# Performance work log

Measured on AMD Instinct MI355X. Metric: run time of the kernel, lower is better.

Reference implementation:

```python
import jax, jax.numpy as jnp
import numpy as np

NUM_ENTITIES = 100000
NUM_RELATIONS = 1000
BATCH = 65536
NUM_NEGS = 64
NUM_TRUE = 1000000


def _hash_triples(t):
    # matches torch: h = e0 << 42 | r << 21 | e2 (ids < 2^21 so no overlap)
    t = t.astype(jnp.int64)
    return (t[:, 0] << 42) | (t[:, 1] << 21) | t[:, 2]


def setup_inputs() -> dict:
    key = jax.random.key(0)
    k1, k2, k3, k4, k5 = jax.random.split(key, 5)
    # positive triples: entities in [1, NUM_ENTITIES), relations in [0, NUM_RELATIONS)
    heads = jax.random.randint(k1, (BATCH,), 1, NUM_ENTITIES, dtype=jnp.int64)
    rels = jax.random.randint(k2, (BATCH,), 0, NUM_RELATIONS, dtype=jnp.int64)
    tails = jax.random.randint(k3, (BATCH,), 1, NUM_ENTITIES, dtype=jnp.int64)
    positive_batch = jnp.stack([heads, rels, tails], axis=1)
    total = BATCH * NUM_NEGS
    # pre-drawn uniform candidates in [1, NUM_ENTITIES) (pad_idx=0 excluded by construction)
    rand_vals = jax.random.randint(k4, (total,), 1, NUM_ENTITIES, dtype=jnp.int64)
    # filter table: sorted unique hashes of training triples (built on host, like buffer init)
    rng = np.random.default_rng(0)
    true = np.stack([
        rng.integers(1, NUM_ENTITIES, NUM_TRUE),
        rng.integers(0, NUM_RELATIONS, NUM_TRUE),
        rng.integers(1, NUM_ENTITIES, NUM_TRUE),
    ], axis=1).astype(np.int64)
    h = (true[:, 0] << 42) | (true[:, 1] << 21) | true[:, 2]
    hashes_sorted = jnp.asarray(np.sort(np.unique(h)))
    return {
        "positive_batch": positive_batch,
        "rand_vals": rand_vals,
        "hashes_sorted": hashes_sorted,
        "num_negs_per_pos": NUM_NEGS,
    }


def reference(positive_batch, rand_vals, hashes_sorted, num_negs_per_pos):
    B = positive_batch.shape[0]
    total = B * num_negs_per_pos
    # repeat_interleave(num_negs, dim=0)
    neg = jnp.repeat(positive_batch, num_negs_per_pos, axis=0)  # [total, 3]
    # corruption scheme [head, tail]: first ceil(total/2) rows corrupt col 0, rest col 2
    split = -(-total // 2)
    col_idx = jnp.where(jnp.arange(total) < split, 0, 2)  # [total]
    orig = jnp.take_along_axis(neg, col_idx[:, None], axis=1)[:, 0]  # [total]
    # pad_idx == 0 fast path: rng in [1, max_index); shift past the original value
    shift = ((rand_vals >= orig) & (orig > 0)).astype(rand_vals.dtype)
    repl = rand_vals + shift
    neg = neg.at[jnp.arange(total), col_idx].set(repl)
    # SortedHashTripleFilter: True = keep (triple not in training set)
    h = _hash_triples(neg)
    L = hashes_sorted.shape[0]
    pos = jnp.searchsorted(hashes_sorted, h)
    in_set = (pos < L) & (hashes_sorted[jnp.clip(pos, 0, L - 1)] == h)
    keep = ~in_set
    return neg.reshape(B, num_negs_per_pos, 3), keep.reshape(B, num_negs_per_pos)
```

## Files before the change

kernel.cpp:

```cpp
#include <hip/hip_runtime.h>

typedef long long i64;
typedef unsigned long long u64;


template <typename T>
__device__ __forceinline__ bool interp_member(const T* __restrict__ table,
                                              int L, u64 key) {
    u64 v0 = (u64)table[0];
    u64 vN = (u64)table[L - 1];
    if (key <= v0) return key == v0;
    if (key >= vN) return key == vN;
    int lo = 0, hi = L - 1;
    u64 vlo = v0, vhi = vN;
    for (int it = 0; it < 12 && hi - lo > 8; ++it) {
        float f = (float)(key - vlo) * __builtin_amdgcn_rcpf((float)(vhi - vlo));
        int mid = lo + (int)(f * (float)(hi - lo));
        if (mid <= lo) mid = lo + 1;
        if (mid >= hi) mid = hi - 1;
        u64 v = (u64)table[mid];
        if (v == key) return true;
        if (v < key) { lo = mid; vlo = v; }
        else         { hi = mid; vhi = v; }
    }
    while (hi - lo > 8) {
        int mid = lo + ((hi - lo) >> 1);
        u64 v = (u64)table[mid];
        if (v == key) return true;
        if (v < key) lo = mid; else hi = mid;
    }
    if constexpr (sizeof(T) == 8) {
        if (L >= 8) {
            int m0 = (lo + 1) & ~1;
            if (m0 > L - 8) m0 = L - 8;
            const ulonglong2* p = (const ulonglong2*)(table + m0);
            ulonglong2 a = p[0];
            ulonglong2 b = p[1];
            ulonglong2 c = p[2];
            ulonglong2 d = p[3];
            return (a.x == key) | (a.y == key) | (b.x == key) | (b.y == key) |
                   (c.x == key) | (c.y == key) | (d.x == key) | (d.y == key);
        }
    }
    bool eq = false;
    for (int j = lo + 1; j < hi; ++j) eq |= ((u64)table[j] == key);
    return eq;
}

template <typename T>
__device__ __forceinline__ void sample_body(
    const T* __restrict__ pos, const T* __restrict__ rand_vals,
    const T* __restrict__ table,
    int* __restrict__ out_neg, int* __restrict__ out_keep,
    unsigned i, int split, int L, unsigned num_negs)
{
    unsigned b = i / num_negs;
    i64 h = (i64)pos[3 * b + 0];
    i64 r = (i64)pos[3 * b + 1];
    i64 t = (i64)pos[3 * b + 2];
    i64 rv = (i64)rand_vals[i];

    const bool corrupt_head = (i < (unsigned)split);
    i64 orig = corrupt_head ? h : t;
    i64 repl = rv + (((rv >= orig) & (orig > 0)) ? 1 : 0);
    if (corrupt_head) h = repl; else t = repl;

    u64 key = ((u64)h << 42) | ((u64)r << 21) | (u64)t;

    out_neg[3 * (size_t)i + 0] = (int)h;
    out_neg[3 * (size_t)i + 1] = (int)r;
    out_neg[3 * (size_t)i + 2] = (int)t;

    bool in_set = interp_member(table, L, key);
    out_keep[i] = in_set ? 0 : 1;
}

__global__ __launch_bounds__(128) void neg_sample_kernel(
    const void* __restrict__ pos, const void* __restrict__ rand_vals,
    const void* __restrict__ table,
    int* __restrict__ out_neg, int* __restrict__ out_keep,
    int total, int split, int L, unsigned num_negs)
{
    unsigned i = blockIdx.x * blockDim.x + threadIdx.x;
    if (i >= (unsigned)total) return;

    const int* pw = (const int*)pos;
    const bool is64 = (pw[3] == 0);

    if (is64) {
        sample_body<i64>((const i64*)pos, (const i64*)rand_vals, (const i64*)table,
                         out_neg, out_keep, i, split, L, num_negs);
    } else {
        sample_body<int>((const int*)pos, (const int*)rand_vals, (const int*)table,
                         out_neg, out_keep, i, split, L, num_negs);
    }
}

extern "C" void kernel_launch(void* const* d_in, const int* in_sizes, int n_in,
                              void* d_out, int out_size, void* d_ws, size_t ws_size,
                              hipStream_t stream) {
    const void* pos       = d_in[0];
    const void* rand_vals = d_in[1];
    const void* table     = d_in[2];

    const int B     = in_sizes[0] / 3;
    const int total = in_sizes[1];
    const int L     = in_sizes[2];
    const unsigned num_negs = (unsigned)(total / B);
    const int split = (total + 1) / 2;

    int* out_neg  = (int*)d_out;
    int* out_keep = out_neg + (size_t)total * 3;

    const int threads = 128;
    const int blocks  = (total + threads - 1) / threads;
    neg_sample_kernel<<<blocks, threads, 0, stream>>>(
        pos, rand_vals, table, out_neg, out_keep, total, split, L, num_negs);
}
```

Measured before the change: 96.58 us.

## Use persistent grid-stride loop with prefetched rand_vals and larger blocks

Replaces the one-thread-per-item launch with a grid capped at 2048 blocks of 256 threads. Each thread loops over items with a grid stride and loads the next rand_vals entry before processing the current one. The aim is to cut launch and block-scheduling overhead and overlap the random-value load with the dependent interpolation-search loads. The trade-off is fewer threads in flight to hide latency of the memory-bound table lookups.

```diff
diff --git a/kernel.cpp b/kernel.cpp
--- a/kernel.cpp
+++ b/kernel.cpp
@@ -48,17 +48,15 @@
 }
 
 template <typename T>
-__device__ __forceinline__ void sample_body(
-    const T* __restrict__ pos, const T* __restrict__ rand_vals,
-    const T* __restrict__ table,
+__device__ __forceinline__ void item_body(
+    const T* __restrict__ pos, const T* __restrict__ table,
     int* __restrict__ out_neg, int* __restrict__ out_keep,
-    unsigned i, int split, int L, unsigned num_negs)
+    unsigned i, i64 rv, int split, int L, unsigned num_negs)
 {
     unsigned b = i / num_negs;
-    i64 h = (i64)pos[3 * b + 0];
-    i64 r = (i64)pos[3 * b + 1];
-    i64 t = (i64)pos[3 * b + 2];
-    i64 rv = (i64)rand_vals[i];
+    i64 h = (i64)pos[3 * (size_t)b + 0];
+    i64 r = (i64)pos[3 * (size_t)b + 1];
+    i64 t = (i64)pos[3 * (size_t)b + 2];
 
     const bool corrupt_head = (i < (unsigned)split);
     i64 orig = corrupt_head ? h : t;
@@ -75,24 +73,44 @@
     out_keep[i] = in_set ? 0 : 1;
 }
 
-__global__ __launch_bounds__(128) void neg_sample_kernel(
+template <typename T>
+__device__ __forceinline__ void persistent_body(
+    const T* __restrict__ pos, const T* __restrict__ rand_vals,
+    const T* __restrict__ table,
+    int* __restrict__ out_neg, int* __restrict__ out_keep,
+    unsigned total, unsigned stride, int split, int L, unsigned num_negs)
+{
+    unsigned i = blockIdx.x * blockDim.x + threadIdx.x;
+    if (i >= total) return;
+
+    i64 rv = (i64)rand_vals[i];
+    for (; i < total; ) {
+        unsigned inext = i + stride;
+        i64 rv_next = 0;
+        if (inext < total) rv_next = (i64)rand_vals[inext];
+        item_body<T>(pos, table, out_neg, out_keep, i, rv, split, L, num_negs);
+        i = inext;
+        rv = rv_next;
+    }
+}
+
+__global__ __launch_bounds__(256) void neg_sample_kernel(
     const void* __restrict__ pos, const void* __restrict__ rand_vals,
     const void* __restrict__ table,
     int* __restrict__ out_neg, int* __restrict__ out_keep,
-    int total, int split, int L, unsigned num_negs)
+    int total, int stride, int split, int L, unsigned num_negs)
 {
-    unsigned i = blockIdx.x * blockDim.x + threadIdx.x;
-    if (i >= (unsigned)total) return;
-
     const int* pw = (const int*)pos;
     const bool is64 = (pw[3] == 0);
 
     if (is64) {
-        sample_body<i64>((const i64*)pos, (const i64*)rand_vals, (const i64*)table,
-                         out_neg, out_keep, i, split, L, num_negs);
+        persistent_body<i64>((const i64*)pos, (const i64*)rand_vals,
+                             (const i64*)table, out_neg, out_keep,
+                             (unsigned)total, (unsigned)stride, split, L, num_negs);
     } else {
-        sample_body<int>((const int*)pos, (const int*)rand_vals, (const int*)table,
-                         out_neg, out_keep, i, split, L, num_negs);
+        persistent_body<int>((const int*)pos, (const int*)rand_vals,
+                             (const int*)table, out_neg, out_keep,
+                             (unsigned)total, (unsigned)stride, split, L, num_negs);
     }
 }
 
@@ -112,8 +130,13 @@
     int* out_neg  = (int*)d_out;
     int* out_keep = out_neg + (size_t)total * 3;
 
-    const int threads = 128;
-    const int blocks  = (total + threads - 1) / threads;
+    const int threads = 256;
+    int blocks = (total + threads - 1) / threads;
+    const int max_blocks = 2048;
+    if (blocks > max_blocks) blocks = max_blocks;
+    const int stride = blocks * threads;
+
     neg_sample_kernel<<<blocks, threads, 0, stream>>>(
-        pos, rand_vals, table, out_neg, out_keep, total, split, L, num_negs);
+        pos, rand_vals, table, out_neg, out_keep, total, stride, split, L,
+        num_negs);
 }
```

After: 96.90 us. About the same (+0.3%).
